# Optimization experiments

Measured on AMD Instinct MI355X. Metric: run time of the kernel, lower is better.

Reference implementation:

```python
import jax, jax.numpy as jnp
import numpy as np

H = 2048   # hidden_size
K = 2048   # key_size
Q = 2048   # query_size
S = 8192   # source sequence length
V = 2048   # value feature dim


def setup_inputs() -> dict:
    key = jax.random.key(0)
    ks = jax.random.split(key, 6)
    query = jax.random.normal(ks[0], (1, 1, Q), dtype=jnp.float32)
    src_key = jax.random.normal(ks[1], (1, S, K), dtype=jnp.float32)
    values = jax.random.normal(ks[2], (S, V), dtype=jnp.float32)
    # nn.Linear weights are [out, in]; all bias-free
    Wq = jax.random.normal(ks[3], (H, Q), dtype=jnp.float32) / np.sqrt(Q)
    Wk = jax.random.normal(ks[4], (H, K), dtype=jnp.float32) / np.sqrt(K)
    Ws = jax.random.normal(ks[5], (1, H), dtype=jnp.float32) / np.sqrt(H)
    return {"query": query, "key": src_key, "values": values,
            "Wq": Wq, "Wk": Wk, "Ws": Ws}


def reference(query, key, values, Wq, Wk, Ws):
    # projected_query: [1,1,H]; projected_key: [1,S,H]
    pq = jnp.einsum('btq,hq->bth', query, Wq)
    pk = jnp.einsum('bsk,hk->bsh', key, Wk)
    # additive (Bahdanau) scores: [1,S,1] -> squeeze(2).unsqueeze(1) -> [1,1,S]
    scores = jnp.einsum('bsh,oh->bso', jnp.tanh(pq + pk), Ws)
    scores = scores[:, :, 0][:, None, :]
    attention_weights = jax.nn.softmax(scores, axis=-1)        # [1,1,S]
    # bmm([1,1,S], values.unsqueeze(0)=[1,S,V]) -> [1,1,V]
    context = jnp.einsum('bts,sv->btv', attention_weights, values)
    return (attention_weights, context)
```

## Files before the change

kernel.cpp:

```cpp
#include <hip/hip_runtime.h>
#include <hip/hip_bf16.h>
#include <math.h>

#define HDIM 2048
#define KDIM 2048
#define SDIM 8192
#define VDIM 2048
#define BKT  64
#define NT   (KDIM / BKT)

using short8 = __attribute__((ext_vector_type(8))) short;
using f32x4  = __attribute__((ext_vector_type(4))) float;
using us8    = __attribute__((ext_vector_type(8))) unsigned short;

typedef const __attribute__((address_space(1))) void g_void;
typedef __attribute__((address_space(3))) void lds_void;

__device__ __forceinline__ unsigned short f2bf(float f) {
  union { float f; unsigned int u; } x; x.f = f;
  unsigned int r = x.u + 0x7fffu + ((x.u >> 16) & 1u);
  return (unsigned short)(r >> 16);
}

__device__ __forceinline__ float tanh_fast(float x) {
  float e = __expf(2.0f * x);
  return 1.0f - 2.0f * __builtin_amdgcn_rcpf(e + 1.0f);
}

__device__ __forceinline__ void barrier_sync() {
  asm volatile("" ::: "memory");
  __builtin_amdgcn_s_barrier();
  asm volatile("" ::: "memory");
}

__global__ __launch_bounds__(256) void cvt_pq_kernel(const float* __restrict__ key,
                                                     const float* __restrict__ Wk,
                                                     unsigned short* __restrict__ outbf,
                                                     const float* __restrict__ query,
                                                     const float* __restrict__ Wq,
                                                     float* __restrict__ pq,
                                                     int keyN8, int cvtBlocks) {
  if ((int)blockIdx.x < cvtBlocks) {
    int i = blockIdx.x * 256 + threadIdx.x;
    const float* src = (i < keyN8) ? &key[(size_t)i * 8] : &Wk[((size_t)i - keyN8) * 8];
    f32x4 a = __builtin_nontemporal_load((const f32x4*)src);
    f32x4 b = __builtin_nontemporal_load((const f32x4*)(src + 4));
    us8 o;
    #pragma unroll
    for (int j = 0; j < 4; ++j) { o[j] = f2bf(a[j]); o[j + 4] = f2bf(b[j]); }
    *(us8*)&outbf[(size_t)i * 8] = o;
  } else {
    int wave = threadIdx.x >> 6, lane = threadIdx.x & 63;
    int h = (blockIdx.x - cvtBlocks) * 4 + wave;
    const float* w = Wq + (size_t)h * KDIM;
    f32x4 s4 = (f32x4)(0.0f);
    #pragma unroll
    for (int i = 0; i < KDIM / 256; ++i) {
      f32x4 q4 = *(const f32x4*)&query[lane * 4 + i * 256];
      f32x4 w4 = __builtin_nontemporal_load((const f32x4*)&w[lane * 4 + i * 256]);
      #pragma unroll
      for (int j = 0; j < 4; ++j) s4[j] = fmaf(q4[j], w4[j], s4[j]);
    }
    float s = s4[0] + s4[1] + s4[2] + s4[3];
    #pragma unroll
    for (int off = 32; off; off >>= 1) s += __shfl_xor(s, off);
    if (lane == 0) pq[h] = s;
  }
}

__global__ __launch_bounds__(512, 2) void scores_kernel(const unsigned short* __restrict__ keybf,
                                                        const unsigned short* __restrict__ wkbf,
                                                        const float* __restrict__ pq,
                                                        const float* __restrict__ Ws,
                                                        float* __restrict__ partial) {
  __shared__ unsigned short lds[65536];

  const int tid = threadIdx.x;
  const int bid = blockIdx.x;
  const int xg = bid & 7, xi = bid >> 3;
  const int bx = xg * 4 + (xi & 3);
  const int by = xi >> 2;
  const int s0 = bx * 256, h0 = by * 256;

  const int wave = tid >> 6, lane = tid & 63;
  const int wm = wave >> 2, wn = wave & 3;
  const int l16 = lane & 15, g16 = lane >> 4;

  const int srow = tid >> 3;
  const int scol = ((tid & 7) * 16) ^ ((srow & 7) << 4);
  const char* aSrc0 = (const char*)keybf + ((size_t)(s0 + srow) * KDIM) * 2 + scol;
  const char* bSrc0 = (const char*)wkbf  + ((size_t)(h0 + srow) * KDIM) * 2 + scol;

  #define STAGE_A(o, kt, buf) __builtin_amdgcn_global_load_lds( \
      (g_void*)(aSrc0 + (size_t)(o) * 64 * KDIM * 2 + (size_t)(kt) * 128), \
      (lds_void*)((char*)lds + (size_t)(buf) * 65536 + (o) * 8192 + wave * 1024), 16, 0, 0)
  #define STAGE_B(o, kt, buf) __builtin_amdgcn_global_load_lds( \
      (g_void*)(bSrc0 + (size_t)(o) * 64 * KDIM * 2 + (size_t)(kt) * 128), \
      (lds_void*)((char*)lds + (size_t)(buf) * 65536 + 32768 + (o) * 8192 + wave * 1024), 16, 0, 0)

  const int xorv = (l16 & 7) << 4;
  int colx[2];
  colx[0] = ((g16 * 16)      ) ^ xorv;
  colx[1] = ((g16 * 16) | 64 ) ^ xorv;
  const int aRowBase = (wm * 128 + l16) * 128;
  const int bRowBase = 32768 + (wn * 64 + l16) * 128;

  f32x4 acc[8][4];
  #pragma unroll
  for (int m = 0; m < 8; ++m)
    #pragma unroll
    for (int n = 0; n < 4; ++n) acc[m][n] = (f32x4)(0.0f);

  STAGE_A(0, 0, 0); STAGE_A(1, 0, 0); STAGE_A(2, 0, 0); STAGE_A(3, 0, 0);
  STAGE_B(0, 0, 0); STAGE_B(1, 0, 0); STAGE_B(2, 0, 0); STAGE_B(3, 0, 0);
  asm volatile("s_waitcnt vmcnt(0)" ::: "memory");
  barrier_sync();

  short8 af[4][2], bf_[4][2];

  for (int t = 0; t < NT; ++t) {
    const int cbase = (t & 1) * 65536;
    const int nbuf = (t & 1) ^ 1;
    const bool more = (t + 1 < NT);

    #pragma unroll
    for (int m = 0; m < 4; ++m)
      #pragma unroll
      for (int ks = 0; ks < 2; ++ks)
        af[m][ks] = *(const short8*)((const char*)lds + cbase + aRowBase + m * 2048 + colx[ks]);
    #pragma unroll
    for (int n = 0; n < 4; ++n)
      #pragma unroll
      for (int ks = 0; ks < 2; ++ks)
        bf_[n][ks] = *(const short8*)((const char*)lds + cbase + bRowBase + n * 2048 + colx[ks]);

    if (more) {
      STAGE_A(0, t + 1, nbuf); STAGE_A(1, t + 1, nbuf);
      STAGE_A(2, t + 1, nbuf); STAGE_A(3, t + 1, nbuf);
      STAGE_B(0, t + 1, nbuf); STAGE_B(1, t + 1, nbuf);
      STAGE_B(2, t + 1, nbuf); STAGE_B(3, t + 1, nbuf);
    }

    __builtin_amdgcn_s_setprio(1);
    #pragma unroll
    for (int ks = 0; ks < 2; ++ks)
      #pragma unroll
      for (int m = 0; m < 4; ++m)
        #pragma unroll
        for (int n = 0; n < 4; ++n)
          acc[m][n] = __builtin_amdgcn_mfma_f32_16x16x32_bf16(af[m][ks], bf_[n][ks], acc[m][n], 0, 0, 0);
    __builtin_amdgcn_s_setprio(0);

    #pragma unroll
    for (int m = 0; m < 4; ++m)
      #pragma unroll
      for (int ks = 0; ks < 2; ++ks)
        af[m][ks] = *(const short8*)((const char*)lds + cbase + aRowBase + (m + 4) * 2048 + colx[ks]);

    __builtin_amdgcn_s_setprio(1);
    #pragma unroll
    for (int ks = 0; ks < 2; ++ks)
      #pragma unroll
      for (int m = 0; m < 4; ++m)
        #pragma unroll
        for (int n = 0; n < 4; ++n)
          acc[m + 4][n] = __builtin_amdgcn_mfma_f32_16x16x32_bf16(af[m][ks], bf_[n][ks], acc[m + 4][n], 0, 0, 0);
    __builtin_amdgcn_s_setprio(0);

    asm volatile("s_waitcnt vmcnt(0)" ::: "memory");
    barrier_sync();
  }

  float pqv[4], wsv[4];
  #pragma unroll
  for (int n = 0; n < 4; ++n) {
    int h = h0 + wn * 64 + n * 16 + l16;
    pqv[n] = pq[h];
    wsv[n] = Ws[h];
  }

  float* sred = (float*)lds;
  #pragma unroll
  for (int m = 0; m < 8; ++m) {
    #pragma unroll
    for (int j = 0; j < 4; ++j) {
      float rs = 0.f;
      #pragma unroll
      for (int n = 0; n < 4; ++n)
        rs += tanh_fast(acc[m][n][j] + pqv[n]) * wsv[n];
      rs += __shfl_xor(rs, 1);
      rs += __shfl_xor(rs, 2);
      rs += __shfl_xor(rs, 4);
      rs += __shfl_xor(rs, 8);
      if (l16 == 0)
        sred[(wm * 128 + m * 16 + g16 * 4 + j) * 4 + wn] = rs;
    }
  }
  __syncthreads();
  if (tid < 256) {
    float v = sred[tid * 4 + 0] + sred[tid * 4 + 1] + sred[tid * 4 + 2] + sred[tid * 4 + 3];
    partial[(size_t)(s0 + tid) * 8 + by] = v;
  }
}

__global__ __launch_bounds__(256) void smax_part_kernel(const float* __restrict__ partial,
                                                        float* __restrict__ wexp,
                                                        float* __restrict__ pairs) {
  __shared__ float red[8];
  int tid = threadIdx.x, wave = tid >> 6, lane = tid & 63;
  int s = blockIdx.x * 256 + tid;
  const float* p = partial + (size_t)s * 8;
  float v = 0.f;
  #pragma unroll
  for (int q = 0; q < 8; ++q) v += p[q];
  float mx = v;
  #pragma unroll
  for (int off = 32; off; off >>= 1) mx = fmaxf(mx, __shfl_xor(mx, off));
  if (lane == 0) red[wave] = mx;
  __syncthreads();
  float bmax = fmaxf(fmaxf(red[0], red[1]), fmaxf(red[2], red[3]));
  float e = __expf(v - bmax);
  wexp[s] = e;
  float sm = e;
  #pragma unroll
  for (int off = 32; off; off >>= 1) sm += __shfl_xor(sm, off);
  if (lane == 0) red[4 + wave] = sm;
  __syncthreads();
  if (tid == 0)
    { pairs[blockIdx.x * 2] = bmax; pairs[blockIdx.x * 2 + 1] = red[4] + red[5] + red[6] + red[7]; }
}

__global__ __launch_bounds__(256) void ctx_fused_kernel(const float* __restrict__ values,
                                                        const float* __restrict__ wexp,
                                                        const float* __restrict__ pairs,
                                                        float* __restrict__ weights,
                                                        float* __restrict__ ctx) {
  __shared__ float scl[32];
  __shared__ f32x4 sred[256];
  int tid = threadIdx.x, b = blockIdx.x;

  float gmax = -1e30f;
  #pragma unroll
  for (int i = 0; i < 32; ++i) gmax = fmaxf(gmax, pairs[2 * i]);
  float gs = 0.f;
  #pragma unroll
  for (int i = 0; i < 32; ++i) gs += pairs[2 * i + 1] * __expf(pairs[2 * i] - gmax);
  if (tid < 32) scl[tid] = __expf(pairs[2 * tid] - gmax);
  __syncthreads();
  float inv = 1.0f / gs;

  if (b < 32) {
    int s = b * 256 + tid;
    weights[s] = wexp[s] * scl[b] * inv;
  }

  const int c4 = b * 2 + (tid & 1);
  const int g  = tid >> 1;
  f32x4 acc = (f32x4)(0.0f);
  for (int s = g; s < SDIM; s += 128) {
    float w = wexp[s] * scl[s >> 8];
    f32x4 v = *(const f32x4*)&values[(size_t)s * VDIM + c4 * 4];
    #pragma unroll
    for (int j = 0; j < 4; ++j) acc[j] = fmaf(w, v[j], acc[j]);
  }
  sred[tid] = acc;
  #pragma unroll
  for (int step = 64; step; step >>= 1) {
    __syncthreads();
    if (g < step) {
      f32x4 a = sred[tid], o = sred[tid + step * 2];
      #pragma unroll
      for (int j = 0; j < 4; ++j) a[j] += o[j];
      sred[tid] = a;
    }
  }
  __syncthreads();
  if (tid < 2) {
    f32x4 a = sred[tid];
    #pragma unroll
    for (int j = 0; j < 4; ++j) a[j] *= inv;
    *(f32x4*)&ctx[(size_t)(b * 2 + tid) * 4] = a;
  }
}

extern "C" void kernel_launch(void* const* d_in, const int* in_sizes, int n_in,
                              void* d_out, int out_size, void* d_ws, size_t ws_size,
                              hipStream_t stream) {
  const float* query  = (const float*)d_in[0];
  const float* key    = (const float*)d_in[1];
  const float* values = (const float*)d_in[2];
  const float* Wq     = (const float*)d_in[3];
  const float* Wk     = (const float*)d_in[4];
  const float* Ws     = (const float*)d_in[5];

  float* out     = (float*)d_out;
  float* weights = out;
  float* ctx     = out + SDIM;

  char* ws = (char*)d_ws;
  unsigned short* keybf = (unsigned short*)ws;
  unsigned short* wkbf  = (unsigned short*)(ws + (size_t)SDIM * KDIM * 2);
  char* tail = ws + (size_t)SDIM * KDIM * 2 + (size_t)HDIM * KDIM * 2;
  float* pq      = (float*)tail;
  float* partial = (float*)(tail + 8192);
  float* wexp    = (float*)(tail + 8192 + (size_t)SDIM * 8 * 4);
  float* pairs   = wexp + SDIM;

  const int keyN8 = SDIM * KDIM / 8;
  const int totN8 = keyN8 + HDIM * KDIM / 8;
  const int cvtBlocks = totN8 / 256;
  cvt_pq_kernel<<<cvtBlocks + HDIM / 4, 256, 0, stream>>>(key, Wk, keybf, query, Wq, pq,
                                                          keyN8, cvtBlocks);
  scores_kernel<<<256, 512, 0, stream>>>(keybf, wkbf, pq, Ws, partial);
  smax_part_kernel<<<32, 256, 0, stream>>>(partial, wexp, pairs);
  ctx_fused_kernel<<<256, 256, 0, stream>>>(values, wexp, pairs, weights, ctx);
}
```

Measured before the change: 126.6 us.

## Restructure score GEMM mainloop into 8-phase ping-pong schedule with split LDS halves

Replaces the simple double-buffered K loop with an unrolled two-tile iteration split into eight phases. Each phase loads a quarter of the A/B fragments from LDS, issues the global-to-LDS copy for the matching half-tile of a future K step, and runs a block of MFMAs, with barriers and partial waitcnts in between. The wave-to-tile mapping changes so waves own interleaved 64-row and 32-column sub-blocks. The aim is to keep memory loads continuously in flight and overlap them with MFMAs instead of waiting for a full tile at every step, at the cost of many more barriers and fragile waitcnt accounting.

New measurement: 126.9 us. Within noise of the previous version (+0.2%).

```diff
diff --git a/kernel.cpp b/kernel.cpp
--- a/kernel.cpp
+++ b/kernel.cpp
@@ -8,6 +8,7 @@
 #define VDIM 2048
 #define BKT  64
 #define NT   (KDIM / BKT)
+#define NITER (NT / 2)
 
 using short8 = __attribute__((ext_vector_type(8))) short;
 using f32x4  = __attribute__((ext_vector_type(4))) float;
@@ -86,24 +87,30 @@
   const int wm = wave >> 2, wn = wave & 3;
   const int l16 = lane & 15, g16 = lane >> 4;
 
-  const int srow = tid >> 3;
-  const int scol = ((tid & 7) * 16) ^ ((srow & 7) << 4);
-  const char* aSrc0 = (const char*)keybf + ((size_t)(s0 + srow) * KDIM) * 2 + scol;
-  const char* bSrc0 = (const char*)wkbf  + ((size_t)(h0 + srow) * KDIM) * 2 + scol;
-
-  #define STAGE_A(o, kt, buf) __builtin_amdgcn_global_load_lds( \
-      (g_void*)(aSrc0 + (size_t)(o) * 64 * KDIM * 2 + (size_t)(kt) * 128), \
-      (lds_void*)((char*)lds + (size_t)(buf) * 65536 + (o) * 8192 + wave * 1024), 16, 0, 0)
-  #define STAGE_B(o, kt, buf) __builtin_amdgcn_global_load_lds( \
-      (g_void*)(bSrc0 + (size_t)(o) * 64 * KDIM * 2 + (size_t)(kt) * 128), \
-      (lds_void*)((char*)lds + (size_t)(buf) * 65536 + 32768 + (o) * 8192 + wave * 1024), 16, 0, 0)
+  const int u = tid >> 3;
+  const int scol = ((tid & 7) * 16) ^ ((u & 7) << 4);
+  const int hi = u >> 5, lo = u & 31;
+  const char* aP = (const char*)keybf + ((size_t)(s0 + u) * KDIM) * 2 + scol;
+  const char* bP = (const char*)wkbf  + ((size_t)(h0 + hi * 64 + lo) * KDIM) * 2 + scol;
+
+  #define STG_A(h, o, kt, db) __builtin_amdgcn_global_load_lds( \
+      (g_void*)(aP + (size_t)((o) * 128 + (h) * 64) * (KDIM * 2) + (size_t)(kt) * 128), \
+      (lds_void*)((char*)lds + (db) + (h) * 16384 + (o) * 8192 + wave * 1024), 16, 0, 0)
+  #define STG_B(h, o, kt, db) __builtin_amdgcn_global_load_lds( \
+      (g_void*)(bP + (size_t)((o) * 128 + (h) * 32) * (KDIM * 2) + (size_t)(kt) * 128), \
+      (lds_void*)((char*)lds + (db) + 32768 + (h) * 16384 + (o) * 8192 + wave * 1024), 16, 0, 0)
 
   const int xorv = (l16 & 7) << 4;
   int colx[2];
   colx[0] = ((g16 * 16)      ) ^ xorv;
   colx[1] = ((g16 * 16) | 64 ) ^ xorv;
-  const int aRowBase = (wm * 128 + l16) * 128;
-  const int bRowBase = 32768 + (wn * 64 + l16) * 128;
+  const int aOff = (64 * wm + l16) * 128;
+  const int bOff = 32768 + (32 * wn + l16) * 128;
+
+  #define LDA0(mm, db, ks) (*(const short8*)((const char*)lds + (db) + aOff + (mm) * 2048 + colx[ks]))
+  #define LDA1(mm, db, ks) (*(const short8*)((const char*)lds + (db) + 16384 + aOff + (mm) * 2048 + colx[ks]))
+  #define LDB0(nn, db, ks) (*(const short8*)((const char*)lds + (db) + bOff + (nn) * 2048 + colx[ks]))
+  #define LDB1(nn, db, ks) (*(const short8*)((const char*)lds + (db) + 16384 + bOff + (nn) * 2048 + colx[ks]))
 
   f32x4 acc[8][4];
   #pragma unroll
@@ -111,63 +118,152 @@
     #pragma unroll
     for (int n = 0; n < 4; ++n) acc[m][n] = (f32x4)(0.0f);
 
-  STAGE_A(0, 0, 0); STAGE_A(1, 0, 0); STAGE_A(2, 0, 0); STAGE_A(3, 0, 0);
-  STAGE_B(0, 0, 0); STAGE_B(1, 0, 0); STAGE_B(2, 0, 0); STAGE_B(3, 0, 0);
-  asm volatile("s_waitcnt vmcnt(0)" ::: "memory");
+  STG_A(0, 0, 0, 0); STG_A(0, 1, 0, 0);
+  STG_B(0, 0, 0, 0); STG_B(0, 1, 0, 0);
+  STG_B(1, 0, 0, 0); STG_B(1, 1, 0, 0);
+  STG_A(1, 0, 0, 0); STG_A(1, 1, 0, 0);
+  STG_A(0, 0, 1, 65536); STG_A(0, 1, 1, 65536);
+  STG_B(0, 0, 1, 65536); STG_B(0, 1, 1, 65536);
+  STG_B(1, 0, 1, 65536); STG_B(1, 1, 1, 65536);
+  asm volatile("s_waitcnt vmcnt(6)" ::: "memory");
   barrier_sync();
 
   short8 af[4][2], bf_[4][2];
 
-  for (int t = 0; t < NT; ++t) {
-    const int cbase = (t & 1) * 65536;
-    const int nbuf = (t & 1) ^ 1;
-    const bool more = (t + 1 < NT);
-
-    #pragma unroll
-    for (int m = 0; m < 4; ++m)
-      #pragma unroll
-      for (int ks = 0; ks < 2; ++ks)
-        af[m][ks] = *(const short8*)((const char*)lds + cbase + aRowBase + m * 2048 + colx[ks]);
-    #pragma unroll
-    for (int n = 0; n < 4; ++n)
-      #pragma unroll
-      for (int ks = 0; ks < 2; ++ks)
-        bf_[n][ks] = *(const short8*)((const char*)lds + cbase + bRowBase + n * 2048 + colx[ks]);
-
-    if (more) {
-      STAGE_A(0, t + 1, nbuf); STAGE_A(1, t + 1, nbuf);
-      STAGE_A(2, t + 1, nbuf); STAGE_A(3, t + 1, nbuf);
-      STAGE_B(0, t + 1, nbuf); STAGE_B(1, t + 1, nbuf);
-      STAGE_B(2, t + 1, nbuf); STAGE_B(3, t + 1, nbuf);
-    }
-
-    __builtin_amdgcn_s_setprio(1);
-    #pragma unroll
-    for (int ks = 0; ks < 2; ++ks)
-      #pragma unroll
-      for (int m = 0; m < 4; ++m)
-        #pragma unroll
-        for (int n = 0; n < 4; ++n)
+  for (int i = 0; i < NITER; ++i) {
+    const int kt0 = 2 * i, kt1 = 2 * i + 1;
+    const bool more = (i + 1 < NITER);
+
+    #pragma unroll
+    for (int m = 0; m < 4; ++m) { af[m][0] = LDA0(m, 0, 0); af[m][1] = LDA0(m, 0, 1); }
+    #pragma unroll
+    for (int n = 0; n < 2; ++n) { bf_[n][0] = LDB0(n, 0, 0); bf_[n][1] = LDB0(n, 0, 1); }
+    STG_A(1, 0, kt1, 65536); STG_A(1, 1, kt1, 65536);
+    asm volatile("s_waitcnt lgkmcnt(8)" ::: "memory");
+    barrier_sync();
+    asm volatile("s_waitcnt lgkmcnt(0)" ::: "memory");
+    __builtin_amdgcn_s_setprio(1);
+    #pragma unroll
+    for (int ks = 0; ks < 2; ++ks)
+      #pragma unroll
+      for (int m = 0; m < 4; ++m)
+        #pragma unroll
+        for (int n = 0; n < 2; ++n)
           acc[m][n] = __builtin_amdgcn_mfma_f32_16x16x32_bf16(af[m][ks], bf_[n][ks], acc[m][n], 0, 0, 0);
     __builtin_amdgcn_s_setprio(0);
-
-    #pragma unroll
-    for (int m = 0; m < 4; ++m)
-      #pragma unroll
-      for (int ks = 0; ks < 2; ++ks)
-        af[m][ks] = *(const short8*)((const char*)lds + cbase + aRowBase + (m + 4) * 2048 + colx[ks]);
-
-    __builtin_amdgcn_s_setprio(1);
-    #pragma unroll
-    for (int ks = 0; ks < 2; ++ks)
-      #pragma unroll
-      for (int m = 0; m < 4; ++m)
-        #pragma unroll
-        for (int n = 0; n < 4; ++n)
+    barrier_sync();
+
+    #pragma unroll
+    for (int n = 2; n < 4; ++n) { bf_[n][0] = LDB1(n - 2, 0, 0); bf_[n][1] = LDB1(n - 2, 0, 1); }
+    if (more) { STG_A(0, 0, kt0 + 2, 0); STG_A(0, 1, kt0 + 2, 0); }
+    barrier_sync();
+    asm volatile("s_waitcnt lgkmcnt(0)" ::: "memory");
+    __builtin_amdgcn_s_setprio(1);
+    #pragma unroll
+    for (int ks = 0; ks < 2; ++ks)
+      #pragma unroll
+      for (int m = 0; m < 4; ++m)
+        #pragma unroll
+        for (int n = 2; n < 4; ++n)
+          acc[m][n] = __builtin_amdgcn_mfma_f32_16x16x32_bf16(af[m][ks], bf_[n][ks], acc[m][n], 0, 0, 0);
+    __builtin_amdgcn_s_setprio(0);
+    barrier_sync();
+
+    #pragma unroll
+    for (int m = 0; m < 4; ++m) { af[m][0] = LDA1(m, 0, 0); af[m][1] = LDA1(m, 0, 1); }
+    if (more) { STG_B(0, 0, kt0 + 2, 0); STG_B(0, 1, kt0 + 2, 0); }
+    barrier_sync();
+    asm volatile("s_waitcnt lgkmcnt(0)" ::: "memory");
+    __builtin_amdgcn_s_setprio(1);
+    #pragma unroll
+    for (int ks = 0; ks < 2; ++ks)
+      #pragma unroll
+      for (int m = 0; m < 4; ++m)
+        #pragma unroll
+        for (int n = 2; n < 4; ++n)
           acc[m + 4][n] = __builtin_amdgcn_mfma_f32_16x16x32_bf16(af[m][ks], bf_[n][ks], acc[m + 4][n], 0, 0, 0);
     __builtin_amdgcn_s_setprio(0);
-
-    asm volatile("s_waitcnt vmcnt(0)" ::: "memory");
+    barrier_sync();
+
+    if (more) { STG_B(1, 0, kt0 + 2, 0); STG_B(1, 1, kt0 + 2, 0); }
+    barrier_sync();
+    __builtin_amdgcn_s_setprio(1);
+    #pragma unroll
+    for (int ks = 0; ks < 2; ++ks)
+      #pragma unroll
+      for (int m = 0; m < 4; ++m)
+        #pragma unroll
+        for (int n = 0; n < 2; ++n)
+          acc[m + 4][n] = __builtin_amdgcn_mfma_f32_16x16x32_bf16(af[m][ks], bf_[n][ks], acc[m + 4][n], 0, 0, 0);
+    __builtin_amdgcn_s_setprio(0);
+    if (more) asm volatile("s_waitcnt vmcnt(6)" ::: "memory");
+    else      asm volatile("s_waitcnt vmcnt(0)" ::: "memory");
+    barrier_sync();
+
+    #pragma unroll
+    for (int m = 0; m < 4; ++m) { af[m][0] = LDA0(m, 65536, 0); af[m][1] = LDA0(m, 65536, 1); }
+    #pragma unroll
+    for (int n = 0; n < 2; ++n) { bf_[n][0] = LDB0(n, 65536, 0); bf_[n][1] = LDB0(n, 65536, 1); }
+    if (more) { STG_A(1, 0, kt0 + 2, 0); STG_A(1, 1, kt0 + 2, 0); }
+    asm volatile("s_waitcnt lgkmcnt(8)" ::: "memory");
+    barrier_sync();
+    asm volatile("s_waitcnt lgkmcnt(0)" ::: "memory");
+    __builtin_amdgcn_s_setprio(1);
+    #pragma unroll
+    for (int ks = 0; ks < 2; ++ks)
+      #pragma unroll
+      for (int m = 0; m < 4; ++m)
+        #pragma unroll
+        for (int n = 0; n < 2; ++n)
+          acc[m][n] = __builtin_amdgcn_mfma_f32_16x16x32_bf16(af[m][ks], bf_[n][ks], acc[m][n], 0, 0, 0);
+    __builtin_amdgcn_s_setprio(0);
+    barrier_sync();
+
+    #pragma unroll
+    for (int n = 2; n < 4; ++n) { bf_[n][0] = LDB1(n - 2, 65536, 0); bf_[n][1] = LDB1(n - 2, 65536, 1); }
+    if (more) { STG_A(0, 0, kt1 + 2, 65536); STG_A(0, 1, kt1 + 2, 65536); }
+    barrier_sync();
+    asm volatile("s_waitcnt lgkmcnt(0)" ::: "memory");
+    __builtin_amdgcn_s_setprio(1);
+    #pragma unroll
+    for (int ks = 0; ks < 2; ++ks)
+      #pragma unroll
+      for (int m = 0; m < 4; ++m)
+        #pragma unroll
+        for (int n = 2; n < 4; ++n)
+          acc[m][n] = __builtin_amdgcn_mfma_f32_16x16x32_bf16(af[m][ks], bf_[n][ks], acc[m][n], 0, 0, 0);
+    __builtin_amdgcn_s_setprio(0);
+    barrier_sync();
+
+    #pragma unroll
+    for (int m = 0; m < 4; ++m) { af[m][0] = LDA1(m, 65536, 0); af[m][1] = LDA1(m, 65536, 1); }
+    if (more) { STG_B(0, 0, kt1 + 2, 65536); STG_B(0, 1, kt1 + 2, 65536); }
+    barrier_sync();
+    asm volatile("s_waitcnt lgkmcnt(0)" ::: "memory");
+    __builtin_amdgcn_s_setprio(1);
+    #pragma unroll
+    for (int ks = 0; ks < 2; ++ks)
+      #pragma unroll
+      for (int m = 0; m < 4; ++m)
+        #pragma unroll
+        for (int n = 2; n < 4; ++n)
+          acc[m + 4][n] = __builtin_amdgcn_mfma_f32_16x16x32_bf16(af[m][ks], bf_[n][ks], acc[m + 4][n], 0, 0, 0);
+    __builtin_amdgcn_s_setprio(0);
+    barrier_sync();
+
+    if (more) { STG_B(1, 0, kt1 + 2, 65536); STG_B(1, 1, kt1 + 2, 65536); }
+    barrier_sync();
+    __builtin_amdgcn_s_setprio(1);
+    #pragma unroll
+    for (int ks = 0; ks < 2; ++ks)
+      #pragma unroll
+      for (int m = 0; m < 4; ++m)
+        #pragma unroll
+        for (int n = 0; n < 2; ++n)
+          acc[m + 4][n] = __builtin_amdgcn_mfma_f32_16x16x32_bf16(af[m][ks], bf_[n][ks], acc[m + 4][n], 0, 0, 0);
+    __builtin_amdgcn_s_setprio(0);
+    if (more) asm volatile("s_waitcnt vmcnt(6)" ::: "memory");
+    else      asm volatile("s_waitcnt vmcnt(0)" ::: "memory");
     barrier_sync();
   }
 
```
